# Performance work log

Hardware: AMD Instinct MI355X
Metric: run time of the kernel (lower is better)

The kernel has to match this reference:

```python
import jax, jax.numpy as jnp
import numpy as np

OUT_F, IN_F = 4096, 4096
N_FREQ = 10000
SCALING = 150.0


def iwht(x):
    """Unnormalized fast Walsh-Hadamard transform along axis 0. x: [n, m], n power of 2."""
    n, m = x.shape
    steps = int(np.log2(n))
    x = x.reshape((2,) * steps + (m,))
    for ax in range(steps):  # log2(n) butterfly stages
        a, b = jnp.split(x, 2, axis=ax)
        x = jnp.concatenate([a + b, a - b], axis=ax)
    return x.reshape(n, m)


def setup_inputs() -> dict:
    key = jax.random.key(0)
    k1, k2, k3, k4 = jax.random.split(key, 4)
    x = jax.random.normal(k1, (2, 512, IN_F), dtype=jnp.float32)
    weight = jax.random.normal(k2, (OUT_F, IN_F), dtype=jnp.float32) * 0.02
    spectrum = jax.random.normal(k3, (N_FREQ,), dtype=jnp.float32)
    indices = jax.random.randint(k4, (2, N_FREQ), 0, OUT_F, dtype=jnp.int64)
    return {"x": x, "weight": weight, "spectrum": spectrum, "indices": indices}


def reference(x, weight, spectrum, indices):
    out_f, in_f = weight.shape
    # sparse scatter of spectrum into dense (out, in) matrix
    dense = jnp.zeros((out_f, in_f), dtype=spectrum.dtype).at[indices[0], indices[1]].set(spectrum)
    # inverse WHT along out axis, scaled
    delta_w = iwht(dense) * (SCALING / np.sqrt(np.float32(out_f)))
    # F.linear(x, base_w + delta_w)
    return jnp.einsum('bsi,oi->bso', x, weight + delta_w.astype(x.dtype))
```

## Files before the change

kernel.cpp:

```cpp
#include <hip/hip_runtime.h>

typedef unsigned short ushort_t;

#define M_DIM 1024
#define N_DIM 4096
#define K_DIM 4096
#define NFREQ 10000
constexpr float SCALE = 150.0f / 64.0f;

typedef __bf16 bf16x8_t  __attribute__((ext_vector_type(8)));
typedef float  f32x16_t  __attribute__((ext_vector_type(16)));

__device__ inline ushort_t f2bf(float f) {
  union { float f; unsigned u; } v; v.f = f;
  unsigned r = v.u + 0x7fffu + ((v.u >> 16) & 1u);
  return (ushort_t)(r >> 16);
}

__global__ __launch_bounds__(256) void build_w4(
    const float* __restrict__ weight,
    const float* __restrict__ spectrum,
    const int* __restrict__ idx,
    const float* __restrict__ x,
    ushort_t* __restrict__ wb,
    ushort_t* __restrict__ xb) {
  if (blockIdx.y == 16) {
    int flat = blockIdx.x * 256 + threadIdx.x;
#pragma unroll 4
    for (int k = 0; k < 64; ++k) {
      int i = flat + k * 16384;
      float4 v = ((const float4*)x)[i];
      ushort4 o;
      o.x = f2bf(v.x); o.y = f2bf(v.y); o.z = f2bf(v.z); o.w = f2bf(v.w);
      ((ushort4*)xb)[i] = o;
    }
    return;
  }

  constexpr int CAP = 1024;
  __shared__ unsigned e_raw[CAP];
  __shared__ float    v_raw[CAP];
  __shared__ uint2    ev_srt[CAP];
  __shared__ int cnt;
  __shared__ int cstart[65];
  __shared__ int coff[64];
  __shared__ int ccnt[64];
  __shared__ unsigned walsh16[16];

  const int tid = threadIdx.x;
  const int ci0 = blockIdx.x * 64;
  const int o0  = blockIdx.y * 256;

  if (tid == 0) cnt = 0;
  if (tid < 64) ccnt[tid] = 0;
  if (tid < 16) {
    unsigned m = tid;
    unsigned w = (m & 1 ? 0xAAAAu : 0u) ^ (m & 2 ? 0xCCCCu : 0u)
               ^ (m & 4 ? 0xF0F0u : 0u) ^ (m & 8 ? 0xFF00u : 0u);
    walsh16[m] = w;
  }
  __syncthreads();

  for (int j = tid; j < NFREQ; j += 256) {
    int c = idx[NFREQ + j];
    if ((c >> 6) == (int)blockIdx.x) {
      int p = atomicAdd(&cnt, 1);
      if (p < CAP) {
        e_raw[p] = ((unsigned)(c & 63) << 26) | ((unsigned)j << 12) | (unsigned)idx[j];
        v_raw[p] = spectrum[j];
        atomicAdd(&ccnt[c & 63], 1);
      }
    }
  }
  __syncthreads();
  const int n = cnt < CAP ? cnt : CAP;

  if (tid < 64) {
    int v = ccnt[tid];
    int s = v;
    for (int d = 1; d < 64; d <<= 1) {
      int o = __shfl_up(s, d, 64);
      if (tid >= d) s += o;
    }
    cstart[tid + 1] = s;
    if (tid == 0) cstart[0] = 0;
    coff[tid] = s - v;
  }
  __syncthreads();
  for (int e = tid; e < n; e += 256) {
    unsigned w = e_raw[e];
    int dc = w >> 26;
    int p = atomicAdd(&coff[dc], 1);
    ev_srt[p] = make_uint2(w, __float_as_uint(v_raw[e]));
  }
  __syncthreads();

  for (int e = tid; e < n; e += 256) {
    uint2 ev = ev_srt[e];
    int dc = ev.x >> 26;
    unsigned r = ev.x & 0xFFFu, j = (ev.x >> 12) & 0x3FFFu;
    int s0 = cstart[dc], e0 = cstart[dc + 1];
    bool dead = false;
    for (int p = s0; p < e0; ++p) {
      unsigned w2 = ev_srt[p].x;
      if ((w2 & 0xFFFu) == r && ((w2 >> 12) & 0x3FFFu) > j) dead = true;
    }
    if (dead) ev_srt[e].y = 0u;
  }
  __syncthreads();

  const int dc0   = (tid & 15) * 4;
  const int rof   = tid >> 4;
  const int obase = o0 + rof * 16;

  float acc[4][16];
#pragma unroll
  for (int c = 0; c < 4; ++c)
#pragma unroll
    for (int j = 0; j < 16; ++j) acc[c][j] = 0.0f;

#pragma unroll
  for (int c = 0; c < 4; ++c) {
    const int s = cstart[dc0 + c], e = cstart[dc0 + c + 1];
    for (int p = s; p < e; ++p) {
      uint2 ev = ev_srt[p];
      unsigned r = ev.x & 0xFFFu;
      unsigned W = walsh16[r & 15u];
      unsigned sx = ev.y ^ ((unsigned)(__popc(obase & r) & 1) << 31);
#pragma unroll
      for (int j = 0; j < 16; ++j) {
        acc[c][j] += __uint_as_float(sx ^ ((W << (31 - j)) & 0x80000000u));
      }
    }
  }

  size_t g = (size_t)obase * K_DIM + ci0 + dc0;
#pragma unroll
  for (int j = 0; j < 16; ++j) {
    float4 w4 = *(const float4*)&weight[g];
    ushort4 ov;
    ov.x = f2bf(w4.x + SCALE * acc[0][j]);
    ov.y = f2bf(w4.y + SCALE * acc[1][j]);
    ov.z = f2bf(w4.z + SCALE * acc[2][j]);
    ov.w = f2bf(w4.w + SCALE * acc[3][j]);
    *(ushort4*)&wb[g] = ov;
    g += K_DIM;
  }
}

__global__ __launch_bounds__(256) void gemm_bt(
    const ushort_t* __restrict__ A,
    const ushort_t* __restrict__ B,
    float* __restrict__ C0,
    float* __restrict__ C1,
    int klen) {
  constexpr int BM = 128, BN = 128, BK = 64;
  __shared__ __align__(16) ushort_t As[BM * BK];
  __shared__ __align__(16) ushort_t Bs[BN * BK];

  const int tid  = threadIdx.x;
  const int wave = tid >> 6, lane = tid & 63;
  const int wrow = wave >> 1, wcol = wave & 1;
  const int l32  = lane & 31, half = lane >> 5;
  const int bm = blockIdx.y * BM, bn = blockIdx.x * BN;
  const int kbeg = blockIdx.z * klen;
  float* __restrict__ dst = blockIdx.z == 0
      ? C0 : C1 + (size_t)(blockIdx.z - 1) * M_DIM * N_DIM;

  const int srow8 = lane >> 3;
  const int sq    = lane & 7;

  f32x16_t acc[2][2] = {};

  for (int kt = kbeg; kt < kbeg + klen; kt += BK) {
#pragma unroll
    for (int c = 0; c < 4; ++c) {
      int ch = wave * 4 + c;
      int gr = ch * 8 + srow8;
      int qg = sq ^ (gr & 7);
      const ushort_t* ga = A + (size_t)(bm + gr) * K_DIM + kt + qg * 8;
      __builtin_amdgcn_global_load_lds(
          (const __attribute__((address_space(1))) void*)ga,
          (__attribute__((address_space(3))) void*)&As[ch * 512], 16, 0, 0);
      const ushort_t* gb = B + (size_t)(bn + gr) * K_DIM + kt + qg * 8;
      __builtin_amdgcn_global_load_lds(
          (const __attribute__((address_space(1))) void*)gb,
          (__attribute__((address_space(3))) void*)&Bs[ch * 512], 16, 0, 0);
    }
    __syncthreads();

    bf16x8_t af[2][4], bfr[2][4];
#pragma unroll
    for (int mi = 0; mi < 2; ++mi) {
#pragma unroll
      for (int h = 0; h < 4; ++h) {
        int q = h * 2 + half;
        int ar = wrow * 64 + mi * 32 + l32;
        af[mi][h]  = *(const bf16x8_t*)&As[ar * BK + ((q ^ (ar & 7)) * 8)];
        int br = wcol * 64 + mi * 32 + l32;
        bfr[mi][h] = *(const bf16x8_t*)&Bs[br * BK + ((q ^ (br & 7)) * 8)];
      }
    }
#pragma unroll
    for (int h = 0; h < 4; ++h)
#pragma unroll
      for (int mi = 0; mi < 2; ++mi)
#pragma unroll
        for (int nj = 0; nj < 2; ++nj)
          acc[mi][nj] = __builtin_amdgcn_mfma_f32_32x32x16_bf16(
              af[mi][h], bfr[nj][h], acc[mi][nj], 0, 0, 0);
    __syncthreads();
  }

#pragma unroll
  for (int mi = 0; mi < 2; ++mi) {
#pragma unroll
    for (int nj = 0; nj < 2; ++nj) {
      int col  = bn + wcol * 64 + nj * 32 + l32;
      int rwb  = bm + wrow * 64 + mi * 32 + 4 * half;
#pragma unroll
      for (int reg = 0; reg < 16; ++reg) {
        int row = rwb + (reg & 3) + 8 * (reg >> 2);
        dst[(size_t)row * N_DIM + col] = acc[mi][nj][reg];
      }
    }
  }
}

__global__ __launch_bounds__(256) void reduce_n(float* __restrict__ out,
                                                const float* __restrict__ part,
                                                int npart) {
  int i = blockIdx.x * 256 + threadIdx.x;
  float4 a = ((const float4*)out)[i];
  for (int t = 0; t < npart; ++t) {
    float4 b = ((const float4*)(part + (size_t)t * M_DIM * N_DIM))[i];
    a.x += b.x; a.y += b.y; a.z += b.z; a.w += b.w;
  }
  ((float4*)out)[i] = a;
}

extern "C" void kernel_launch(void* const* d_in, const int* in_sizes, int n_in,
                              void* d_out, int out_size, void* d_ws, size_t ws_size,
                              hipStream_t stream) {
  const float* x        = (const float*)d_in[0];
  const float* weight   = (const float*)d_in[1];
  const float* spectrum = (const float*)d_in[2];
  const int*   indices  = (const int*)d_in[3];
  float* out = (float*)d_out;

  char* ws = (char*)d_ws;
  const size_t WB_BYTES = (size_t)N_DIM * K_DIM * 2;
  const size_t XB_BYTES = (size_t)M_DIM * K_DIM * 2;
  const size_t P1_BYTES = (size_t)M_DIM * N_DIM * 4;

  ushort_t* wb = (ushort_t*)ws;
  ushort_t* xb = (ushort_t*)(ws + WB_BYTES);
  float* part = (float*)(ws + WB_BYTES + XB_BYTES);

  int zsplit = (ws_size >= WB_BYTES + XB_BYTES + P1_BYTES) ? 2 : 1;

  build_w4<<<dim3(64, 17), 256, 0, stream>>>(weight, spectrum, indices, x, wb, xb);

  gemm_bt<<<dim3(N_DIM / 128, M_DIM / 128, zsplit), 256, 0, stream>>>(
      xb, wb, out, part, K_DIM / zsplit);
  if (zsplit > 1)
    reduce_n<<<(M_DIM * N_DIM / 4) / 256, 256, 0, stream>>>(out, part, zsplit - 1);
}
```

Before: 185.6 us.

## Store GEMM LDS tiles in MFMA fragment order and spread x conversion over more blocks

```diff
diff --git a/kernel.cpp b/kernel.cpp
--- a/kernel.cpp
+++ b/kernel.cpp
@@ -24,11 +24,11 @@
     const float* __restrict__ x,
     ushort_t* __restrict__ wb,
     ushort_t* __restrict__ xb) {
-  if (blockIdx.y == 16) {
-    int flat = blockIdx.x * 256 + threadIdx.x;
+  if (blockIdx.y >= 16) {
+    int b = (blockIdx.y - 16) * 64 + blockIdx.x;
 #pragma unroll 4
-    for (int k = 0; k < 64; ++k) {
-      int i = flat + k * 16384;
+    for (int k = 0; k < 16; ++k) {
+      int i = b * 4096 + k * 256 + threadIdx.x;
       float4 v = ((const float4*)x)[i];
       ushort4 o;
       o.x = f2bf(v.x); o.y = f2bf(v.y); o.z = f2bf(v.z); o.w = f2bf(v.w);
@@ -167,25 +167,21 @@
   float* __restrict__ dst = blockIdx.z == 0
       ? C0 : C1 + (size_t)(blockIdx.z - 1) * M_DIM * N_DIM;
 
-  const int srow8 = lane >> 3;
-  const int sq    = lane & 7;
+  const ushort_t* garow = A + (size_t)(bm + wave * 32 + l32) * K_DIM + half * 8;
+  const ushort_t* gbrow = B + (size_t)(bn + wave * 32 + l32) * K_DIM + half * 8;
 
   f32x16_t acc[2][2] = {};
 
   for (int kt = kbeg; kt < kbeg + klen; kt += BK) {
 #pragma unroll
     for (int c = 0; c < 4; ++c) {
-      int ch = wave * 4 + c;
-      int gr = ch * 8 + srow8;
-      int qg = sq ^ (gr & 7);
-      const ushort_t* ga = A + (size_t)(bm + gr) * K_DIM + kt + qg * 8;
+      int g = wave * 4 + c;
       __builtin_amdgcn_global_load_lds(
-          (const __attribute__((address_space(1))) void*)ga,
-          (__attribute__((address_space(3))) void*)&As[ch * 512], 16, 0, 0);
-      const ushort_t* gb = B + (size_t)(bn + gr) * K_DIM + kt + qg * 8;
+          (const __attribute__((address_space(1))) void*)(garow + kt + c * 16),
+          (__attribute__((address_space(3))) void*)&As[g * 512], 16, 0, 0);
       __builtin_amdgcn_global_load_lds(
-          (const __attribute__((address_space(1))) void*)gb,
-          (__attribute__((address_space(3))) void*)&Bs[ch * 512], 16, 0, 0);
+          (const __attribute__((address_space(1))) void*)(gbrow + kt + c * 16),
+          (__attribute__((address_space(3))) void*)&Bs[g * 512], 16, 0, 0);
     }
     __syncthreads();
 
@@ -194,11 +190,8 @@
     for (int mi = 0; mi < 2; ++mi) {
 #pragma unroll
       for (int h = 0; h < 4; ++h) {
-        int q = h * 2 + half;
-        int ar = wrow * 64 + mi * 32 + l32;
-        af[mi][h]  = *(const bf16x8_t*)&As[ar * BK + ((q ^ (ar & 7)) * 8)];
-        int br = wcol * 64 + mi * 32 + l32;
-        bfr[mi][h] = *(const bf16x8_t*)&Bs[br * BK + ((q ^ (br & 7)) * 8)];
+        af[mi][h]  = *(const bf16x8_t*)&As[((wrow * 2 + mi) * 4 + h) * 512 + lane * 8];
+        bfr[mi][h] = *(const bf16x8_t*)&Bs[((wcol * 2 + mi) * 4 + h) * 512 + lane * 8];
       }
     }
 #pragma unroll
@@ -259,7 +252,7 @@
 
   int zsplit = (ws_size >= WB_BYTES + XB_BYTES + P1_BYTES) ? 2 : 1;
 
-  build_w4<<<dim3(64, 17), 256, 0, stream>>>(weight, spectrum, indices, x, wb, xb);
+  build_w4<<<dim3(64, 20), 256, 0, stream>>>(weight, spectrum, indices, x, wb, xb);
 
   gemm_bt<<<dim3(N_DIM / 128, M_DIM / 128, zsplit), 256, 0, stream>>>(
       xb, wb, out, part, K_DIM / zsplit);
```

After: 219.5 us. +18.3%, slower.
